# Kernel optimization log

Measured on AMD Instinct MI355X. Metric: run time of the kernel, lower is better.

Reference implementation:

```python
import jax, jax.numpy as jnp
import numpy as np

NEG_SLOPE = 0.2  # PyG GATConv default


def gat_conv(x, edge_index, W, att_src, att_dst, bias, heads, out_c, concat):
    """One PyG-style GATConv layer (eval mode, add_self_loops=True)."""
    N = x.shape[0]
    loop = jnp.arange(N, dtype=edge_index.dtype)
    src = jnp.concatenate([edge_index[0], loop])  # [E+N]
    dst = jnp.concatenate([edge_index[1], loop])
    h = (x @ W).reshape(N, heads, out_c)                     # [N,H,C]
    a_src = jnp.einsum('nhc,hc->nh', h, att_src)             # [N,H]
    a_dst = jnp.einsum('nhc,hc->nh', h, att_dst)
    e = jax.nn.leaky_relu(a_src[src] + a_dst[dst], NEG_SLOPE)  # [E+N,H]
    # segment softmax over incoming edges of each dst node (self-loops guarantee non-empty segments)
    emax = jax.ops.segment_max(e, dst, num_segments=N)
    e = jnp.exp(e - emax[dst])
    denom = jax.ops.segment_sum(e, dst, num_segments=N)
    alpha = e / denom[dst]                                   # [E+N,H]
    msg = h[src] * alpha[:, :, None]                         # [E+N,H,C]
    out = jax.ops.segment_sum(msg, dst, num_segments=N)      # [N,H,C]
    out = out.reshape(N, heads * out_c) if concat else out.mean(axis=1)
    return out + bias


def setup_inputs() -> dict:
    key = jax.random.key(0)
    ks = jax.random.split(key, 10)
    N, E, Fin, Hc, H, Out = 20000, 320000, 256, 128, 4, 256
    s = lambda k, shp: jax.random.normal(k, shp, dtype=jnp.float32) * 0.05
    return {
        'x': jax.random.normal(ks[0], (N, Fin), dtype=jnp.float32),
        'edge_index': jax.random.randint(ks[1], (2, E), 0, N, dtype=jnp.int64),
        'W1': s(ks[2], (Fin, H * Hc)),
        'att_src1': s(ks[3], (H, Hc)),
        'att_dst1': s(ks[4], (H, Hc)),
        'b1': s(ks[5], (H * Hc,)),
        'W2': s(ks[6], (H * Hc, Out)),
        'att_src2': s(ks[7], (1, Out)),
        'att_dst2': s(ks[8], (1, Out)),
        'b2': s(ks[9], (Out,)),
    }


def reference(x, edge_index, W1, att_src1, att_dst1, b1, W2, att_src2, att_dst2, b2):
    h = gat_conv(x, edge_index, W1, att_src1, att_dst1, b1, heads=4, out_c=128, concat=True)
    h = jax.nn.gelu(h, approximate=False)  # torch.nn.GELU default is exact
    out = gat_conv(h, edge_index, W2, att_src2, att_dst2, b2, heads=1, out_c=256, concat=False)
    return out
```

## Files before the change

kernel.cpp:

```cpp
#include <hip/hip_runtime.h>
#include <hip/hip_bf16.h>

#define NODES 20000
#define EDGES 320000
#define FIN   256
#define HEADS 4
#define C1    128
#define F1    512
#define F2    256
#define TOT_E (EDGES + NODES)

typedef __bf16 bf16x8 __attribute__((ext_vector_type(8)));
typedef float  f32x4  __attribute__((ext_vector_type(4)));
typedef unsigned short ushort_t;
typedef ushort_t ushx8 __attribute__((ext_vector_type(8)));

__device__ __forceinline__ float bf2f(ushort_t u) {
    union { unsigned int i; float f; } c; c.i = ((unsigned)u) << 16; return c.f;
}
__device__ __forceinline__ ushort_t f2bf(float f) {
    union { float f; unsigned int i; } c; c.f = f;
    unsigned r = (c.i + 0x7fffu + ((c.i >> 16) & 1u)) >> 16;
    return (ushort_t)r;
}
__device__ __forceinline__ float lrelu(float v) { return (v > 0.f) ? v : 0.2f * v; }

__global__ void k_cast_bf16(const float* __restrict__ in, ushort_t* __restrict__ out, int n) {
    int i = (blockIdx.x * blockDim.x + threadIdx.x) * 4;
    if (i >= n) return;
    float4 v = *reinterpret_cast<const float4*>(in + i);
    ushort4 o;
    o.x = f2bf(v.x); o.y = f2bf(v.y); o.z = f2bf(v.z); o.w = f2bf(v.w);
    *reinterpret_cast<ushort4*>(out + i) = o;
}

__global__ void k_transpose_bf16(const float* __restrict__ in, ushort_t* __restrict__ out, int K, int N) {
    int idx = blockIdx.x * blockDim.x + threadIdx.x;
    if (idx >= K * N) return;
    int n = idx / K, k = idx % K;
    out[idx] = f2bf(in[k * N + n]);
}

__global__ void k_hist(const int* __restrict__ ei, int* __restrict__ counts) {
    int e = blockIdx.x * blockDim.x + threadIdx.x;
    if (e >= TOT_E) return;
    int dst = (e < EDGES) ? ei[EDGES + e] : (e - EDGES);
    atomicAdd(&counts[dst], 1);
}

__global__ void k_scan(const int* __restrict__ counts, int* __restrict__ offsets, int* __restrict__ cursor) {
    __shared__ int wsum[16];
    const int PT = 20;
    int tid = threadIdx.x;
    int lane = tid & 63, wv = tid >> 6;
    int base = tid * PT;
    int v[PT];
    int tsum = 0;
    #pragma unroll
    for (int i = 0; i < PT; i++) {
        int idx = base + i;
        v[i] = (idx < NODES) ? counts[idx] : 0;
        tsum += v[i];
    }
    int orig = tsum;
    for (int o = 1; o < 64; o <<= 1) {
        int t = __shfl_up(tsum, o);
        if (lane >= o) tsum += t;
    }
    if (lane == 63) wsum[wv] = tsum;
    __syncthreads();
    if (wv == 0 && lane < 16) {
        int s = wsum[lane];
        for (int o = 1; o < 16; o <<= 1) {
            int t = __shfl_up(s, o);
            if (lane >= o) s += t;
        }
        wsum[lane] = s;
    }
    __syncthreads();
    int wpre = (wv == 0) ? 0 : wsum[wv - 1];
    int excl = wpre + tsum - orig;
    #pragma unroll
    for (int i = 0; i < PT; i++) {
        int idx = base + i;
        if (idx < NODES) { offsets[idx] = excl; cursor[idx] = excl; }
        excl += v[i];
    }
}

__global__ void k_scatter(const int* __restrict__ ei, int* __restrict__ cursor, int* __restrict__ csr_src) {
    int e = blockIdx.x * blockDim.x + threadIdx.x;
    if (e >= TOT_E) return;
    int src, dst;
    if (e < EDGES) { src = ei[e]; dst = ei[EDGES + e]; }
    else           { src = dst = e - EDGES; }
    int pos = atomicAdd(&cursor[dst], 1);
    csr_src[pos] = src;
}

__launch_bounds__(256)
__global__ void k_gemm_bf16(const ushort_t* __restrict__ A, const ushort_t* __restrict__ Bt,
                            ushort_t* __restrict__ Cbf, int M, int N, int K) {
    __shared__ ushort_t lA[128 * 72];
    __shared__ ushort_t lB[128 * 72];
    const int tid  = threadIdx.x;
    const int lane = tid & 63, w = tid >> 6;
    const int wr = w >> 1, wc = w & 1;
    const int row0 = blockIdx.x * 128;
    const int col0 = blockIdx.y * 128;
    f32x4 acc[4][4] = {};

    for (int k0 = 0; k0 < K; k0 += 64) {
        for (int p = 0; p < 4; p++) {
            int t  = p * 256 + tid;
            int r  = t >> 3;
            int kc = (t & 7) * 8;
            ushx8 va = {};
            int ga = row0 + r;
            if (ga < M) va = *reinterpret_cast<const ushx8*>(&A[(size_t)ga * K + k0 + kc]);
            *reinterpret_cast<ushx8*>(&lA[r * 72 + kc]) = va;
            ushx8 vb = *reinterpret_cast<const ushx8*>(&Bt[(size_t)(col0 + r) * K + k0 + kc]);
            *reinterpret_cast<ushx8*>(&lB[r * 72 + kc]) = vb;
        }
        __syncthreads();
        for (int kk = 0; kk < 2; kk++) {
            int kb = kk * 32 + (lane >> 4) * 8;
            bf16x8 af[4], bfr[4];
            for (int m = 0; m < 4; m++)
                af[m] = *reinterpret_cast<const bf16x8*>(&lA[(wr * 64 + m * 16 + (lane & 15)) * 72 + kb]);
            for (int n = 0; n < 4; n++)
                bfr[n] = *reinterpret_cast<const bf16x8*>(&lB[(wc * 64 + n * 16 + (lane & 15)) * 72 + kb]);
            for (int m = 0; m < 4; m++)
                for (int n = 0; n < 4; n++)
                    acc[m][n] = __builtin_amdgcn_mfma_f32_16x16x32_bf16(af[m], bfr[n], acc[m][n], 0, 0, 0);
        }
        __syncthreads();
    }

    for (int m = 0; m < 4; m++) {
        int gr0 = row0 + wr * 64 + m * 16 + (lane >> 4) * 4;
        for (int n = 0; n < 4; n++) {
            int gc = col0 + wc * 64 + n * 16 + (lane & 15);
            for (int r = 0; r < 4; r++) {
                int gr = gr0 + r;
                if (gr < M) Cbf[(size_t)gr * N + gc] = f2bf(acc[m][n][r]);
            }
        }
    }
}

__global__ void k_attsc1(const ushort_t* __restrict__ h1, const float* __restrict__ att_src,
                         const float* __restrict__ att_dst, float* __restrict__ a_src,
                         float* __restrict__ a_dst) {
    int n = blockIdx.x;
    int h = threadIdx.x >> 6, lane = threadIdx.x & 63;
    unsigned hv = *reinterpret_cast<const unsigned*>(&h1[(size_t)n * F1 + h * C1 + lane * 2]);
    float x0 = bf2f((ushort_t)(hv & 0xffff)), x1 = bf2f((ushort_t)(hv >> 16));
    const float* as = att_src + h * C1 + lane * 2;
    const float* ad = att_dst + h * C1 + lane * 2;
    float ds = x0 * as[0] + x1 * as[1];
    float dd = x0 * ad[0] + x1 * ad[1];
    for (int off = 32; off; off >>= 1) { ds += __shfl_xor(ds, off); dd += __shfl_xor(dd, off); }
    if (lane == 0) { a_src[n * HEADS + h] = ds; a_dst[n * HEADS + h] = dd; }
}

__global__ void k_attsc2(const ushort_t* __restrict__ h2, const float* __restrict__ att_src,
                         const float* __restrict__ att_dst, float* __restrict__ a_src,
                         float* __restrict__ a_dst) {
    int w = threadIdx.x >> 6, lane = threadIdx.x & 63;
    int n = blockIdx.x * 4 + w;
    ushort4 hv = *reinterpret_cast<const ushort4*>(&h2[(size_t)n * F2 + lane * 4]);
    float x0 = bf2f(hv.x), x1 = bf2f(hv.y), x2 = bf2f(hv.z), x3 = bf2f(hv.w);
    float4 as = *reinterpret_cast<const float4*>(att_src + lane * 4);
    float4 ad = *reinterpret_cast<const float4*>(att_dst + lane * 4);
    float ds = x0 * as.x + x1 * as.y + x2 * as.z + x3 * as.w;
    float dd = x0 * ad.x + x1 * ad.y + x2 * ad.z + x3 * ad.w;
    for (int off = 32; off; off >>= 1) { ds += __shfl_xor(ds, off); dd += __shfl_xor(dd, off); }
    if (lane == 0) { a_src[n] = ds; a_dst[n] = dd; }
}

__launch_bounds__(256)
__global__ void k_agg1(const ushort_t* __restrict__ h1, const int* __restrict__ offsets,
                       const int* __restrict__ counts, const int* __restrict__ csr,
                       const float* __restrict__ a_src, const float* __restrict__ a_dst,
                       const float* __restrict__ b1, ushort_t* __restrict__ hgelu) {
    int w = threadIdx.x >> 6, lane = threadIdx.x & 63;
    int d = blockIdx.x * 4 + w;
    int h = lane >> 4;
    int off = offsets[d], deg = counts[d];
    float adst = a_dst[d * HEADS + h];
    float acc[8] = {};
    float den = 0.f;
    int j = 0;
    for (; j + 4 <= deg; j += 4) {
        int s0 = csr[off + j + 0];
        int s1 = csr[off + j + 1];
        int s2 = csr[off + j + 2];
        int s3 = csr[off + j + 3];
        ushx8 v0 = *reinterpret_cast<const ushx8*>(&h1[(size_t)s0 * F1 + lane * 8]);
        ushx8 v1 = *reinterpret_cast<const ushx8*>(&h1[(size_t)s1 * F1 + lane * 8]);
        ushx8 v2 = *reinterpret_cast<const ushx8*>(&h1[(size_t)s2 * F1 + lane * 8]);
        ushx8 v3 = *reinterpret_cast<const ushx8*>(&h1[(size_t)s3 * F1 + lane * 8]);
        float w0 = __expf(lrelu(a_src[s0 * HEADS + h] + adst));
        float w1 = __expf(lrelu(a_src[s1 * HEADS + h] + adst));
        float w2 = __expf(lrelu(a_src[s2 * HEADS + h] + adst));
        float w3 = __expf(lrelu(a_src[s3 * HEADS + h] + adst));
        den += (w0 + w1) + (w2 + w3);
        #pragma unroll
        for (int i = 0; i < 8; i++)
            acc[i] += w0 * bf2f(v0[i]) + w1 * bf2f(v1[i]) + w2 * bf2f(v2[i]) + w3 * bf2f(v3[i]);
    }
    for (; j < deg; j++) {
        int s = csr[off + j];
        ushx8 hv = *reinterpret_cast<const ushx8*>(&h1[(size_t)s * F1 + lane * 8]);
        float wgt = __expf(lrelu(a_src[s * HEADS + h] + adst));
        den += wgt;
        #pragma unroll
        for (int i = 0; i < 8; i++) acc[i] += wgt * bf2f(hv[i]);
    }
    float inv = 1.f / den;
    int c0 = lane * 8;
    ushx8 o;
    #pragma unroll
    for (int i = 0; i < 8; i++) {
        float v = acc[i] * inv + b1[c0 + i];
        v = 0.5f * v * (1.f + erff(v * 0.70710678118654752f));
        o[i] = f2bf(v);
    }
    *reinterpret_cast<ushx8*>(&hgelu[(size_t)d * F1 + c0]) = o;
}

__launch_bounds__(256)
__global__ void k_agg2(const ushort_t* __restrict__ h2, const int* __restrict__ offsets,
                       const int* __restrict__ counts, const int* __restrict__ csr,
                       const float* __restrict__ a_src, const float* __restrict__ a_dst,
                       const float* __restrict__ b2, float* __restrict__ out) {
    int w = threadIdx.x >> 6, lane = threadIdx.x & 63;
    int d = blockIdx.x * 4 + w;
    int off = offsets[d], deg = counts[d];
    int half = lane >> 5, il = lane & 31;
    float adst = a_dst[d];
    float acc[8] = {};
    float den = 0.f;
    int j = 0;
    for (; j + 8 <= deg; j += 8) {
        int s0 = csr[off + j + 0 + half];
        int s1 = csr[off + j + 2 + half];
        int s2 = csr[off + j + 4 + half];
        int s3 = csr[off + j + 6 + half];
        ushx8 v0 = *reinterpret_cast<const ushx8*>(&h2[(size_t)s0 * F2 + il * 8]);
        ushx8 v1 = *reinterpret_cast<const ushx8*>(&h2[(size_t)s1 * F2 + il * 8]);
        ushx8 v2 = *reinterpret_cast<const ushx8*>(&h2[(size_t)s2 * F2 + il * 8]);
        ushx8 v3 = *reinterpret_cast<const ushx8*>(&h2[(size_t)s3 * F2 + il * 8]);
        float w0 = __expf(lrelu(a_src[s0] + adst));
        float w1 = __expf(lrelu(a_src[s1] + adst));
        float w2 = __expf(lrelu(a_src[s2] + adst));
        float w3 = __expf(lrelu(a_src[s3] + adst));
        den += (w0 + w1) + (w2 + w3);
        #pragma unroll
        for (int i = 0; i < 8; i++)
            acc[i] += w0 * bf2f(v0[i]) + w1 * bf2f(v1[i]) + w2 * bf2f(v2[i]) + w3 * bf2f(v3[i]);
    }
    for (; j < deg; j += 2) {
        int jj = j + half;
        if (jj < deg) {
            int s = csr[off + jj];
            ushx8 hv = *reinterpret_cast<const ushx8*>(&h2[(size_t)s * F2 + il * 8]);
            float wgt = __expf(lrelu(a_src[s] + adst));
            den += wgt;
            #pragma unroll
            for (int i = 0; i < 8; i++) acc[i] += wgt * bf2f(hv[i]);
        }
    }
    den += __shfl_xor(den, 32);
    #pragma unroll
    for (int i = 0; i < 8; i++) acc[i] += __shfl_xor(acc[i], 32);
    if (half == 0) {
        float inv = 1.f / den;
        int c0 = il * 8;
        float4 o0, o1;
        o0.x = acc[0] * inv + b2[c0 + 0];
        o0.y = acc[1] * inv + b2[c0 + 1];
        o0.z = acc[2] * inv + b2[c0 + 2];
        o0.w = acc[3] * inv + b2[c0 + 3];
        o1.x = acc[4] * inv + b2[c0 + 4];
        o1.y = acc[5] * inv + b2[c0 + 5];
        o1.z = acc[6] * inv + b2[c0 + 6];
        o1.w = acc[7] * inv + b2[c0 + 7];
        *reinterpret_cast<float4*>(&out[(size_t)d * F2 + c0])     = o0;
        *reinterpret_cast<float4*>(&out[(size_t)d * F2 + c0 + 4]) = o1;
    }
}

extern "C" void kernel_launch(void* const* d_in, const int* in_sizes, int n_in,
                              void* d_out, int out_size, void* d_ws, size_t ws_size,
                              hipStream_t stream) {
    const float* x        = (const float*)d_in[0];
    const int*   ei       = (const int*)d_in[1];
    const float* W1       = (const float*)d_in[2];
    const float* att_src1 = (const float*)d_in[3];
    const float* att_dst1 = (const float*)d_in[4];
    const float* b1       = (const float*)d_in[5];
    const float* W2       = (const float*)d_in[6];
    const float* att_src2 = (const float*)d_in[7];
    const float* att_dst2 = (const float*)d_in[8];
    const float* b2       = (const float*)d_in[9];
    float* out = (float*)d_out;

    char* p = (char*)d_ws;
    auto alloc = [&](size_t bytes) -> char* {
        char* r = p; p += (bytes + 255) & ~(size_t)255; return r;
    };
    ushort_t* x_bf  = (ushort_t*)alloc((size_t)NODES * FIN * 2);
    ushort_t* w1t   = (ushort_t*)alloc((size_t)F1 * FIN * 2);
    ushort_t* w2t   = (ushort_t*)alloc((size_t)F2 * F1 * 2);
    ushort_t* h1    = (ushort_t*)alloc((size_t)NODES * F1 * 2);
    ushort_t* hg    = (ushort_t*)alloc((size_t)NODES * F1 * 2);
    ushort_t* h2    = (ushort_t*)alloc((size_t)NODES * F2 * 2);
    float* as1      = (float*)alloc((size_t)NODES * HEADS * 4);
    float* ad1      = (float*)alloc((size_t)NODES * HEADS * 4);
    float* as2      = (float*)alloc((size_t)NODES * 4);
    float* ad2      = (float*)alloc((size_t)NODES * 4);
    int* counts     = (int*)alloc((size_t)NODES * 4);
    int* offsets    = (int*)alloc((size_t)NODES * 4);
    int* cursor     = (int*)alloc((size_t)NODES * 4);
    int* csr        = (int*)alloc((size_t)TOT_E * 4);

    hipMemsetAsync(counts, 0, NODES * 4, stream);
    k_cast_bf16<<<(NODES * FIN / 4 + 255) / 256, 256, 0, stream>>>(x, x_bf, NODES * FIN);
    k_transpose_bf16<<<(FIN * F1 + 255) / 256, 256, 0, stream>>>(W1, w1t, FIN, F1);
    k_transpose_bf16<<<(F1 * F2 + 255) / 256, 256, 0, stream>>>(W2, w2t, F1, F2);
    k_hist<<<(TOT_E + 255) / 256, 256, 0, stream>>>(ei, counts);
    k_scan<<<1, 1024, 0, stream>>>(counts, offsets, cursor);
    k_scatter<<<(TOT_E + 255) / 256, 256, 0, stream>>>(ei, cursor, csr);

    k_gemm_bf16<<<dim3(157, 4), 256, 0, stream>>>(x_bf, w1t, h1, NODES, F1, FIN);
    k_attsc1<<<NODES, 256, 0, stream>>>(h1, att_src1, att_dst1, as1, ad1);
    k_agg1<<<NODES / 4, 256, 0, stream>>>(h1, offsets, counts, csr, as1, ad1, b1, hg);

    k_gemm_bf16<<<dim3(157, 2), 256, 0, stream>>>(hg, w2t, h2, NODES, F2, F1);
    k_attsc2<<<NODES / 4, 256, 0, stream>>>(h2, att_src2, att_dst2, as2, ad2);
    k_agg2<<<NODES / 4, 256, 0, stream>>>(h2, offsets, counts, csr, as2, ad2, b2, out);
}
```

Baseline: 288.8 us.

## Fuse attention-score dots into GEMM epilogue, merge prep kernels, use direct global-to-LDS loads

Removes the separate attention-score kernels: the GEMM epilogue now does per-row dot products with att_src/att_dst from the accumulators. It reduces them across lanes with shuffles and atomically adds partial sums per column tile into zeroed buffers. The x cast and the two weight transposes are merged into one prep kernel, and the memset now zeroes counts and score buffers in one call. GEMM tile staging switches to global_load_lds with an unpadded 64-element LDS stride and no row bounds check, which saves register traffic but may cause LDS bank conflicts and reads past the last row into neighbouring workspace.

```diff
diff --git a/kernel.cpp b/kernel.cpp
--- a/kernel.cpp
+++ b/kernel.cpp
@@ -15,6 +15,10 @@
 typedef unsigned short ushort_t;
 typedef ushort_t ushx8 __attribute__((ext_vector_type(8)));
 
+#define GLOAD_LDS16(gp, lp) \
+    __builtin_amdgcn_global_load_lds((const __attribute__((address_space(1))) void*)(gp), \
+                                     (__attribute__((address_space(3))) void*)(lp), 16, 0, 0)
+
 __device__ __forceinline__ float bf2f(ushort_t u) {
     union { unsigned int i; float f; } c; c.i = ((unsigned)u) << 16; return c.f;
 }
@@ -25,20 +29,28 @@
 }
 __device__ __forceinline__ float lrelu(float v) { return (v > 0.f) ? v : 0.2f * v; }
 
-__global__ void k_cast_bf16(const float* __restrict__ in, ushort_t* __restrict__ out, int n) {
-    int i = (blockIdx.x * blockDim.x + threadIdx.x) * 4;
-    if (i >= n) return;
-    float4 v = *reinterpret_cast<const float4*>(in + i);
-    ushort4 o;
-    o.x = f2bf(v.x); o.y = f2bf(v.y); o.z = f2bf(v.z); o.w = f2bf(v.w);
-    *reinterpret_cast<ushort4*>(out + i) = o;
-}
-
-__global__ void k_transpose_bf16(const float* __restrict__ in, ushort_t* __restrict__ out, int K, int N) {
-    int idx = blockIdx.x * blockDim.x + threadIdx.x;
-    if (idx >= K * N) return;
-    int n = idx / K, k = idx % K;
-    out[idx] = f2bf(in[k * N + n]);
+#define CAST_T (NODES * FIN / 4)
+#define T1N    (FIN * F1)
+#define T2N    (F1 * F2)
+__global__ void k_prep(const float* __restrict__ x, ushort_t* __restrict__ x_bf,
+                       const float* __restrict__ W1, ushort_t* __restrict__ w1t,
+                       const float* __restrict__ W2, ushort_t* __restrict__ w2t) {
+    int t = blockIdx.x * 256 + threadIdx.x;
+    if (t < CAST_T) {
+        int i = t * 4;
+        float4 v = *reinterpret_cast<const float4*>(x + i);
+        ushort4 o;
+        o.x = f2bf(v.x); o.y = f2bf(v.y); o.z = f2bf(v.z); o.w = f2bf(v.w);
+        *reinterpret_cast<ushort4*>(x_bf + i) = o;
+    } else if (t < CAST_T + T1N) {
+        int idx = t - CAST_T;
+        int n = idx >> 8, k = idx & 255;
+        w1t[idx] = f2bf(W1[k * F1 + n]);
+    } else if (t < CAST_T + T1N + T2N) {
+        int idx = t - CAST_T - T1N;
+        int n = idx >> 9, k = idx & 511;
+        w2t[idx] = f2bf(W2[k * F2 + n]);
+    }
 }
 
 __global__ void k_hist(const int* __restrict__ ei, int* __restrict__ counts) {
@@ -99,10 +111,12 @@
 }
 
 __launch_bounds__(256)
-__global__ void k_gemm_bf16(const ushort_t* __restrict__ A, const ushort_t* __restrict__ Bt,
-                            ushort_t* __restrict__ Cbf, int M, int N, int K) {
-    __shared__ ushort_t lA[128 * 72];
-    __shared__ ushort_t lB[128 * 72];
+__global__ void k_gemm_att(const ushort_t* __restrict__ A, const ushort_t* __restrict__ Bt,
+                           ushort_t* __restrict__ Cbf, int M, int N, int K,
+                           const float* __restrict__ attS, const float* __restrict__ attD,
+                           float* __restrict__ aS, float* __restrict__ aD, int aStride) {
+    __shared__ ushort_t lA[128 * 64];
+    __shared__ ushort_t lB[128 * 64];
     const int tid  = threadIdx.x;
     const int lane = tid & 63, w = tid >> 6;
     const int wr = w >> 1, wc = w & 1;
@@ -110,73 +124,88 @@
     const int col0 = blockIdx.y * 128;
     f32x4 acc[4][4] = {};
 
+    const int srow = lane >> 3;
+    const int scol = (lane & 7) * 8;
+
     for (int k0 = 0; k0 < K; k0 += 64) {
+        #pragma unroll
         for (int p = 0; p < 4; p++) {
-            int t  = p * 256 + tid;
-            int r  = t >> 3;
-            int kc = (t & 7) * 8;
-            ushx8 va = {};
-            int ga = row0 + r;
-            if (ga < M) va = *reinterpret_cast<const ushx8*>(&A[(size_t)ga * K + k0 + kc]);
-            *reinterpret_cast<ushx8*>(&lA[r * 72 + kc]) = va;
-            ushx8 vb = *reinterpret_cast<const ushx8*>(&Bt[(size_t)(col0 + r) * K + k0 + kc]);
-            *reinterpret_cast<ushx8*>(&lB[r * 72 + kc]) = vb;
+            int rb = p * 32 + w * 8;
+            GLOAD_LDS16(&A[(size_t)(row0 + rb + srow) * K + k0 + scol], &lA[rb * 64]);
+            GLOAD_LDS16(&Bt[(size_t)(col0 + rb + srow) * K + k0 + scol], &lB[rb * 64]);
         }
         __syncthreads();
+        #pragma unroll
         for (int kk = 0; kk < 2; kk++) {
             int kb = kk * 32 + (lane >> 4) * 8;
             bf16x8 af[4], bfr[4];
+            #pragma unroll
             for (int m = 0; m < 4; m++)
-                af[m] = *reinterpret_cast<const bf16x8*>(&lA[(wr * 64 + m * 16 + (lane & 15)) * 72 + kb]);
+                af[m] = *reinterpret_cast<const bf16x8*>(&lA[(wr * 64 + m * 16 + (lane & 15)) * 64 + kb]);
+            #pragma unroll
             for (int n = 0; n < 4; n++)
-                bfr[n] = *reinterpret_cast<const bf16x8*>(&lB[(wc * 64 + n * 16 + (lane & 15)) * 72 + kb]);
+                bfr[n] = *reinterpret_cast<const bf16x8*>(&lB[(wc * 64 + n * 16 + (lane & 15)) * 64 + kb]);
+            #pragma unroll
             for (int m = 0; m < 4; m++)
+                #pragma unroll
                 for (int n = 0; n < 4; n++)
                     acc[m][n] = __builtin_amdgcn_mfma_f32_16x16x32_bf16(af[m], bfr[n], acc[m][n], 0, 0, 0);
         }
         __syncthreads();
     }
 
+    #pragma unroll
     for (int m = 0; m < 4; m++) {
         int gr0 = row0 + wr * 64 + m * 16 + (lane >> 4) * 4;
+        #pragma unroll
         for (int n = 0; n < 4; n++) {
             int gc = col0 + wc * 64 + n * 16 + (lane & 15);
+            #pragma unroll
             for (int r = 0; r < 4; r++) {
                 int gr = gr0 + r;
                 if (gr < M) Cbf[(size_t)gr * N + gc] = f2bf(acc[m][n][r]);
             }
         }
     }
-}
-
-__global__ void k_attsc1(const ushort_t* __restrict__ h1, const float* __restrict__ att_src,
-                         const float* __restrict__ att_dst, float* __restrict__ a_src,
-                         float* __restrict__ a_dst) {
-    int n = blockIdx.x;
-    int h = threadIdx.x >> 6, lane = threadIdx.x & 63;
-    unsigned hv = *reinterpret_cast<const unsigned*>(&h1[(size_t)n * F1 + h * C1 + lane * 2]);
-    float x0 = bf2f((ushort_t)(hv & 0xffff)), x1 = bf2f((ushort_t)(hv >> 16));
-    const float* as = att_src + h * C1 + lane * 2;
-    const float* ad = att_dst + h * C1 + lane * 2;
-    float ds = x0 * as[0] + x1 * as[1];
-    float dd = x0 * ad[0] + x1 * ad[1];
-    for (int off = 32; off; off >>= 1) { ds += __shfl_xor(ds, off); dd += __shfl_xor(dd, off); }
-    if (lane == 0) { a_src[n * HEADS + h] = ds; a_dst[n * HEADS + h] = dd; }
-}
-
-__global__ void k_attsc2(const ushort_t* __restrict__ h2, const float* __restrict__ att_src,
-                         const float* __restrict__ att_dst, float* __restrict__ a_src,
-                         float* __restrict__ a_dst) {
-    int w = threadIdx.x >> 6, lane = threadIdx.x & 63;
-    int n = blockIdx.x * 4 + w;
-    ushort4 hv = *reinterpret_cast<const ushort4*>(&h2[(size_t)n * F2 + lane * 4]);
-    float x0 = bf2f(hv.x), x1 = bf2f(hv.y), x2 = bf2f(hv.z), x3 = bf2f(hv.w);
-    float4 as = *reinterpret_cast<const float4*>(att_src + lane * 4);
-    float4 ad = *reinterpret_cast<const float4*>(att_dst + lane * 4);
-    float ds = x0 * as.x + x1 * as.y + x2 * as.z + x3 * as.w;
-    float dd = x0 * ad.x + x1 * ad.y + x2 * ad.z + x3 * ad.w;
-    for (int off = 32; off; off >>= 1) { ds += __shfl_xor(ds, off); dd += __shfl_xor(dd, off); }
-    if (lane == 0) { a_src[n] = ds; a_dst[n] = dd; }
+
+    float pds[16], pdd[16];
+    #pragma unroll
+    for (int i = 0; i < 16; i++) { pds[i] = 0.f; pdd[i] = 0.f; }
+    const int attBase = blockIdx.y * 128;
+    #pragma unroll
+    for (int n = 0; n < 4; n++) {
+        int colr = wc * 64 + n * 16 + (lane & 15);
+        float av = attS[attBase + colr];
+        float dv = attD[attBase + colr];
+        #pragma unroll
+        for (int m = 0; m < 4; m++)
+            #pragma unroll
+            for (int r = 0; r < 4; r++) {
+                pds[m * 4 + r] += acc[m][n][r] * av;
+                pdd[m * 4 + r] += acc[m][n][r] * dv;
+            }
+    }
+    #pragma unroll
+    for (int o = 1; o < 16; o <<= 1) {
+        #pragma unroll
+        for (int i = 0; i < 16; i++) {
+            pds[i] += __shfl_xor(pds[i], o);
+            pdd[i] += __shfl_xor(pdd[i], o);
+        }
+    }
+    if ((lane & 15) == 0) {
+        int hoff = (aStride == HEADS) ? blockIdx.y : 0;
+        #pragma unroll
+        for (int m = 0; m < 4; m++)
+            #pragma unroll
+            for (int r = 0; r < 4; r++) {
+                int gr = row0 + wr * 64 + m * 16 + (lane >> 4) * 4 + r;
+                if (gr < M) {
+                    atomicAdd(&aS[gr * aStride + hoff], pds[m * 4 + r]);
+                    atomicAdd(&aD[gr * aStride + hoff], pdd[m * 4 + r]);
+                }
+            }
+    }
 }
 
 __launch_bounds__(256)
@@ -317,28 +346,28 @@
     ushort_t* h1    = (ushort_t*)alloc((size_t)NODES * F1 * 2);
     ushort_t* hg    = (ushort_t*)alloc((size_t)NODES * F1 * 2);
     ushort_t* h2    = (ushort_t*)alloc((size_t)NODES * F2 * 2);
+    char* zbase     = p;
+    int* counts     = (int*)alloc((size_t)NODES * 4);
     float* as1      = (float*)alloc((size_t)NODES * HEADS * 4);
     float* ad1      = (float*)alloc((size_t)NODES * HEADS * 4);
     float* as2      = (float*)alloc((size_t)NODES * 4);
     float* ad2      = (float*)alloc((size_t)NODES * 4);
-    int* counts     = (int*)alloc((size_t)NODES * 4);
+    size_t zspan    = (size_t)(p - zbase);
     int* offsets    = (int*)alloc((size_t)NODES * 4);
     int* cursor     = (int*)alloc((size_t)NODES * 4);
     int* csr        = (int*)alloc((size_t)TOT_E * 4);
 
-    hipMemsetAsync(counts, 0, NODES * 4, stream);
-    k_cast_bf16<<<(NODES * FIN / 4 + 255) / 256, 256, 0, stream>>>(x, x_bf, NODES * FIN);
-    k_transpose_bf16<<<(FIN * F1 + 255) / 256, 256, 0, stream>>>(W1, w1t, FIN, F1);
-    k_transpose_bf16<<<(F1 * F2 + 255) / 256, 256, 0, stream>>>(W2, w2t, F1, F2);
+    hipMemsetAsync(zbase, 0, zspan, stream);
+    k_prep<<<(CAST_T + T1N + T2N + 255) / 256, 256, 0, stream>>>(x, x_bf, W1, w1t, W2, w2t);
     k_hist<<<(TOT_E + 255) / 256, 256, 0, stream>>>(ei, counts);
     k_scan<<<1, 1024, 0, stream>>>(counts, offsets, cursor);
     k_scatter<<<(TOT_E + 255) / 256, 256, 0, stream>>>(ei, cursor, csr);
 
-    k_gemm_bf16<<<dim3(157, 4), 256, 0, stream>>>(x_bf, w1t, h1, NODES, F1, FIN);
-    k_attsc1<<<NODES, 256, 0, stream>>>(h1, att_src1, att_dst1, as1, ad1);
+    k_gemm_att<<<dim3(157, 4), 256, 0, stream>>>(x_bf, w1t, h1, NODES, F1, FIN,
+                                                 att_src1, att_dst1, as1, ad1, HEADS);
     k_agg1<<<NODES / 4, 256, 0, stream>>>(h1, offsets, counts, csr, as1, ad1, b1, hg);
 
-    k_gemm_bf16<<<dim3(157, 2), 256, 0, stream>>>(hg, w2t, h2, NODES, F2, F1);
-    k_attsc2<<<NODES / 4, 256, 0, stream>>>(h2, att_src2, att_dst2, as2, ad2);
+    k_gemm_att<<<dim3(157, 2), 256, 0, stream>>>(hg, w2t, h2, NODES, F2, F1,
+                                                 att_src2, att_dst2, as2, ad2, 1);
     k_agg2<<<NODES / 4, 256, 0, stream>>>(h2, offsets, counts, csr, as2, ad2, b2, out);
 }
```

Measured after the change: 289.1 us. Within noise of the previous version (+0.1%).
